# Performance work log

Hardware: AMD Instinct MI355X
Metric: run time of the kernel (lower is better)

The kernel has to match this reference:

```python
import jax, jax.numpy as jnp
import numpy as np

V_PER_MESH = 6596
HIDDEN = 128
# per-body-part clamp limits from the original module (parts 1..14)
LIMITS = jnp.array([0.04, 0.06, 0.04, 0.04, 0.02, 0.02, 0.04, 0.04,
                    0.03, 0.03, 0.02, 0.02, 0.01, 0.01], dtype=jnp.float32)


def setup_inputs() -> dict:
    key = jax.random.key(0)
    ks = jax.random.split(key, 16)
    B, V, H = 32, V_PER_MESH, HIDDEN
    N = B * V
    E = 3 * N
    inp = {}
    inp["verts"] = jax.random.normal(ks[0], (N, 3), jnp.float32)
    inp["normals"] = jax.random.normal(ks[1], (N, 3), jnp.float32)
    inp["anchor_v"] = jax.random.uniform(ks[2], (V, 3), jnp.float32)
    inp["edges"] = jax.random.randint(ks[3], (E, 2), 0, N)
    inp["part_id"] = jax.random.randint(ks[4], (V,), 0, 14)
    dims = [3, H + 3, H + 3]  # first gconv sees only vert normals (vert_feat_dim=0)
    i = 5
    for l, d in enumerate(dims):
        s = 1.0 / np.sqrt(d)
        inp[f"w0_{l}"] = jax.random.normal(ks[i], (d, H), jnp.float32) * s; i += 1
        inp[f"b0_{l}"] = jnp.zeros((H,), jnp.float32)
        inp[f"w1_{l}"] = jax.random.normal(ks[i], (d, H), jnp.float32) * s; i += 1
        inp[f"b1_{l}"] = jnp.zeros((H,), jnp.float32)
    inp["w_off"] = jax.random.normal(ks[i], (H + 3, 3), jnp.float32) * 0.01
    inp["b_off"] = jnp.zeros((3,), jnp.float32)
    return inp


def _forward(verts, normals, anchor_v, edges, part_id, layers, w_off, b_off):
    N = verts.shape[0]
    B = N // V_PER_MESH
    e0, e1 = edges[:, 0], edges[:, 1]
    feats = normals  # vert_pos_packed (verts_normals_packed), vert_feats=None
    for (w0, b0, w1, b1) in layers:
        x0 = feats @ w0 + b0            # [N,H] self transform
        x1 = feats @ w1 + b1            # [N,H] neighbor transform
        # undirected gather-scatter over mesh edges
        nbr = jnp.zeros_like(x0).at[e0].add(x1[e1]).at[e1].add(x1[e0])
        h = jax.nn.relu(x0 + nbr)       # vert_feats_nopos
        feats = jnp.concatenate([h, normals], axis=1)  # [N,H+3]
    deform = jnp.tanh(feats @ w_off + b_off)  # [N,3]
    # per-body-part clamp, vectorized: one limit per vertex, tiled over meshes
    lim = jnp.tile(LIMITS[part_id], B)[:, None]          # [N,1]
    clamped = jnp.clip(deform, -lim, lim)
    anchor = jnp.tile(anchor_v, (B, 1))                  # [N,3]
    new_verts = verts + clamped * anchor                 # offset_verts
    return new_verts, h


def reference(verts, normals, anchor_v, edges, part_id,
              w0_0, b0_0, w1_0, b1_0,
              w0_1, b0_1, w1_1, b1_1,
              w0_2, b0_2, w1_2, b1_2,
              w_off, b_off):
    layers = [(w0_0, b0_0, w1_0, b1_0),
              (w0_1, b0_1, w1_1, b1_1),
              (w0_2, b0_2, w1_2, b1_2)]
    return _forward(verts, normals, anchor_v, edges, part_id, layers, w_off, b_off)
```

## Files before the change

kernel.cpp:

```cpp
#include <hip/hip_runtime.h>

#define N_TOT 211072
#define V_MESH 6596
#define E_TOT 633216
#define CAP 32
#define KP 184
#define KSTEPS 5

typedef __attribute__((ext_vector_type(8))) short bf16x8;
typedef __attribute__((ext_vector_type(4))) float f32x4;

__constant__ float c_LIM[14] = {0.04f,0.06f,0.04f,0.04f,0.02f,0.02f,0.04f,0.04f,
                                0.03f,0.03f,0.02f,0.02f,0.01f,0.01f};

__device__ __forceinline__ unsigned f2bf(float f) {
    unsigned x = __float_as_uint(f);
    return (x + 0x7fffu + ((x >> 16) & 1u)) >> 16;
}
__device__ __forceinline__ float bflo(unsigned u) { return __uint_as_float(u << 16); }
__device__ __forceinline__ float bfhi(unsigned u) { return __uint_as_float(u & 0xffff0000u); }
__device__ __forceinline__ unsigned cvt_pk_bf16(float lo, float hi) {
    unsigned r;
    asm("v_cvt_pk_bf16_f32 %0, %1, %2" : "=v"(r) : "v"(lo), "v"(hi));
    return r;
}

__global__ __launch_bounds__(256) void fill_adj_kernel(const int* __restrict__ edges,
                                                       int* __restrict__ cnt,
                                                       int* __restrict__ adj) {
    int e = blockIdx.x * 256 + threadIdx.x;
    if (e >= E_TOT) return;
    int2 ed = ((const int2*)edges)[e];
    int p0 = atomicAdd(&cnt[ed.x], 1);
    if (p0 < CAP) adj[(size_t)ed.x * CAP + p0] = ed.y;
    int p1 = atomicAdd(&cnt[ed.y], 1);
    if (p1 < CAP) adj[(size_t)ed.y * CAP + p1] = ed.x;
}

__global__ __launch_bounds__(256) void pad_adj_kernel(const int* __restrict__ cnt,
                                                      int* __restrict__ adj) {
    int i = blockIdx.x * 256 + threadIdx.x;
    if (i >= N_TOT) return;
    int deg = cnt[i]; if (deg > CAP) deg = CAP;
    for (int k = deg; k < CAP; ++k) adj[(size_t)i * CAP + k] = N_TOT;
}

__global__ __launch_bounds__(256) void prep_nrm4_kernel(const float* __restrict__ normals,
                                                        float4* __restrict__ nrm4) {
    int i = blockIdx.x * 256 + threadIdx.x;
    if (i > N_TOT) return;
    float4 v = {0.f, 0.f, 0.f, 0.f};
    if (i < N_TOT) {
        v.x = normals[(size_t)i * 3 + 0];
        v.y = normals[(size_t)i * 3 + 1];
        v.z = normals[(size_t)i * 3 + 2];
    }
    nrm4[i] = v;
}

__global__ __launch_bounds__(256) void nsum_kernel(const float4* __restrict__ nrm4,
                                                   const int* __restrict__ cnt,
                                                   const int* __restrict__ adj,
                                                   float4* __restrict__ SS) {
    int i = blockIdx.x * 256 + threadIdx.x;
    if (i >= N_TOT) return;
    int deg = cnt[i]; if (deg > CAP) deg = CAP;
    const int4* a4 = (const int4*)(adj + (size_t)i * CAP);
    int4 A = a4[0], B = a4[1];
    float4 n0 = nrm4[A.x], n1 = nrm4[A.y], n2 = nrm4[A.z], n3 = nrm4[A.w];
    float4 m0 = nrm4[B.x], m1 = nrm4[B.y], m2 = nrm4[B.z], m3 = nrm4[B.w];
    float sx = ((n0.x + n1.x) + (n2.x + n3.x)) + ((m0.x + m1.x) + (m2.x + m3.x));
    float sy = ((n0.y + n1.y) + (n2.y + n3.y)) + ((m0.y + m1.y) + (m2.y + m3.y));
    float sz = ((n0.z + n1.z) + (n2.z + n3.z)) + ((m0.z + m1.z) + (m2.z + m3.z));
    for (int bq = 8; bq < deg; bq += 8) {
        int4 C = a4[bq / 4], D = a4[bq / 4 + 1];
        float4 p0 = nrm4[C.x], p1 = nrm4[C.y], p2 = nrm4[C.z], p3 = nrm4[C.w];
        float4 q0 = nrm4[D.x], q1 = nrm4[D.y], q2 = nrm4[D.z], q3 = nrm4[D.w];
        sx += ((p0.x + p1.x) + (p2.x + p3.x)) + ((q0.x + q1.x) + (q2.x + q3.x));
        sy += ((p0.y + p1.y) + (p2.y + p3.y)) + ((q0.y + q1.y) + (q2.y + q3.y));
        sz += ((p0.z + p1.z) + (p2.z + p3.z)) + ((q0.z + q1.z) + (q2.z + q3.z));
    }
    float4 out; out.x = sx; out.y = sy; out.z = sz; out.w = (float)deg;
    SS[i] = out;
}

__global__ __launch_bounds__(256) void conv_w_kernel(const float* __restrict__ w0,
                                                     const float* __restrict__ b0,
                                                     const float* __restrict__ w1,
                                                     const float* __restrict__ b1,
                                                     short* __restrict__ Wt,
                                                     float* __restrict__ bb) {
    int c = blockIdx.x;
    int k = threadIdx.x;
    const float* w = (c < 128) ? w0 : w1;
    int cc = c & 127;
    if (k < KP) {
        unsigned val = (k < 131) ? f2bf(w[(size_t)k * 128 + cc]) : 0u;
        Wt[(size_t)c * KP + k] = (short)val;
    }
    if (k == 0) bb[c] = (c < 128) ? b0[cc] : b1[cc];
}

__global__ __launch_bounds__(1024, 8) void fused1_kernel(const float4* __restrict__ nrm4,
                                                         const float4* __restrict__ SS,
                                                         const float* __restrict__ w0,
                                                         const float* __restrict__ b0,
                                                         const float* __restrict__ w1,
                                                         const float* __restrict__ b1,
                                                         const short* __restrict__ Wt,
                                                         const float* __restrict__ bb,
                                                         unsigned* __restrict__ xc_out) {
    __shared__ short tileA[16 * KP];
    __shared__ short tileC[16 * 256];
    __shared__ float wL[2][3][128];
    __shared__ float bL[2][128];

    int tid  = threadIdx.x;
    int w    = tid >> 6;
    int lane = tid & 63;
    int g    = lane >> 4;
    int ln   = lane & 15;
    int row0 = blockIdx.x * 16;
    int i    = row0 + w;

    if (tid < 768) {
        int mm = tid / 384, r = tid - mm * 384;
        (&wL[mm][0][0])[r] = (mm ? w1 : w0)[r];
    } else {
        int t2 = tid - 768;
        if (t2 < 256) bL[t2 >> 7][t2 & 127] = ((t2 >> 7) ? b1 : b0)[t2 & 127];
    }

    float4 self4 = nrm4[i];
    float4 S4 = SS[i];
    float degf = S4.w;
    __syncthreads();

    int c0 = 2 * lane, c1 = 2 * lane + 1;
    float h0 = bL[0][c0] + degf * bL[1][c0]
             + self4.x * wL[0][0][c0] + self4.y * wL[0][1][c0] + self4.z * wL[0][2][c0]
             + S4.x * wL[1][0][c0] + S4.y * wL[1][1][c0] + S4.z * wL[1][2][c0];
    float h1 = bL[0][c1] + degf * bL[1][c1]
             + self4.x * wL[0][0][c1] + self4.y * wL[0][1][c1] + self4.z * wL[0][2][c1]
             + S4.x * wL[1][0][c1] + S4.y * wL[1][1][c1] + S4.z * wL[1][2][c1];
    h0 = fmaxf(h0, 0.f);
    h1 = fmaxf(h1, 0.f);

    unsigned* tA32 = (unsigned*)tileA;
    tA32[w * (KP / 2) + lane] = cvt_pk_bf16(h0, h1);
    if (lane < 16) {
        unsigned v = (lane == 0) ? cvt_pk_bf16(self4.x, self4.y)
                   : (lane == 1) ? cvt_pk_bf16(self4.z, 0.f) : 0u;
        tA32[w * (KP / 2) + 64 + lane] = v;
    }
    __syncthreads();

    int cb = w * 16;
    float bv = bb[cb + ln];
    f32x4 acc = {bv, bv, bv, bv};
    #pragma unroll
    for (int kk = 0; kk < KSTEPS; ++kk) {
        bf16x8 bf = *(const bf16x8*)(Wt + (size_t)(cb + ln) * KP + kk * 32 + g * 8);
        bf16x8 af = *(const bf16x8*)(tileA + ln * KP + kk * 32 + g * 8);
        acc = __builtin_amdgcn_mfma_f32_16x16x32_bf16(af, bf, acc, 0, 0, 0);
    }
    #pragma unroll
    for (int j = 0; j < 4; ++j) {
        float po = __shfl_xor(acc[j], 1);
        if (!(ln & 1)) {
            unsigned pk = cvt_pk_bf16(acc[j], po);
            int dd = w * 8 + (ln >> 1);
            int row = g * 4 + j;
            ((unsigned*)tileC)[row * 128 + (dd ^ (g << 3))] = pk;
        }
    }
    __syncthreads();

    int key = (w >> 2) << 3;
    ushort4 v4 = *(const ushort4*)&((unsigned*)tileC)[w * 128 + ((2 * lane) ^ key)];
    ((ushort4*)(xc_out + (size_t)(row0 + w) * 128))[lane] = v4;
}

__global__ __launch_bounds__(1024, 8) void fused_kernel(const unsigned* __restrict__ xc_in,
                                                        const float4* __restrict__ nrm4,
                                                        const int* __restrict__ cnt,
                                                        const int* __restrict__ adj,
                                                        const short* __restrict__ Wt,
                                                        const float* __restrict__ bb,
                                                        unsigned* __restrict__ xc_out) {
    __shared__ short tileA[16 * KP];
    __shared__ short tileC[16 * 256];
    int tid  = threadIdx.x;
    int w    = tid >> 6;
    int lane = tid & 63;
    int g    = lane >> 4;
    int ln   = lane & 15;
    int row0 = blockIdx.x * 16;
    int i    = row0 + w;

    int deg0 = cnt[i];
    int jv = (lane < CAP) ? adj[(size_t)i * CAP + lane] : (int)N_TOT;

    const unsigned* x1b = xc_in + 64 + lane;
    unsigned u[8];
    #pragma unroll
    for (int q = 0; q < 8; ++q) {
        int j = __builtin_amdgcn_readlane(jv, q);
        u[q] = x1b[(size_t)j * 128];
    }
    unsigned selfu = xc_in[(size_t)i * 128 + lane];
    float4 self4 = nrm4[i];
    int cb = w * 16;
    float bv = bb[cb + ln];
    bf16x8 bfrag[KSTEPS];
    #pragma unroll
    for (int kk = 0; kk < KSTEPS; ++kk)
        bfrag[kk] = *(const bf16x8*)(Wt + (size_t)(cb + ln) * KP + kk * 32 + g * 8);

    float a0 = bflo(selfu), a1 = bfhi(selfu);
    float d0 = 0.f, d1 = 0.f;
    #pragma unroll
    for (int q = 0; q < 8; q += 2) {
        a0 += bflo(u[q]);     a1 += bfhi(u[q]);
        d0 += bflo(u[q + 1]); d1 += bfhi(u[q + 1]);
    }
    int deg = (deg0 > CAP) ? CAP : deg0;
    deg = __builtin_amdgcn_readfirstlane(deg);
    for (int bq = 8; bq < deg; bq += 8) {
        unsigned v[8];
        #pragma unroll
        for (int q = 0; q < 8; ++q) {
            int j = __builtin_amdgcn_readlane(jv, bq + q);
            v[q] = x1b[(size_t)j * 128];
        }
        #pragma unroll
        for (int q = 0; q < 8; q += 2) {
            a0 += bflo(v[q]);     a1 += bfhi(v[q]);
            d0 += bflo(v[q + 1]); d1 += bfhi(v[q + 1]);
        }
    }
    a0 = fmaxf(a0 + d0, 0.f);
    a1 = fmaxf(a1 + d1, 0.f);

    unsigned* tA32 = (unsigned*)tileA;
    tA32[w * (KP / 2) + lane] = cvt_pk_bf16(a0, a1);
    if (lane < 16) {
        unsigned v = (lane == 0) ? cvt_pk_bf16(self4.x, self4.y)
                   : (lane == 1) ? cvt_pk_bf16(self4.z, 0.f) : 0u;
        tA32[w * (KP / 2) + 64 + lane] = v;
    }
    __syncthreads();

    f32x4 acc = {bv, bv, bv, bv};
    #pragma unroll
    for (int kk = 0; kk < KSTEPS; ++kk) {
        bf16x8 af = *(const bf16x8*)(tileA + ln * KP + kk * 32 + g * 8);
        acc = __builtin_amdgcn_mfma_f32_16x16x32_bf16(af, bfrag[kk], acc, 0, 0, 0);
    }
    #pragma unroll
    for (int j = 0; j < 4; ++j) {
        float po = __shfl_xor(acc[j], 1);
        if (!(ln & 1)) {
            unsigned pk = cvt_pk_bf16(acc[j], po);
            int dd = w * 8 + (ln >> 1);
            int row = g * 4 + j;
            ((unsigned*)tileC)[row * 128 + (dd ^ (g << 3))] = pk;
        }
    }
    __syncthreads();

    int key = (w >> 2) << 3;
    ushort4 v4 = *(const ushort4*)&((unsigned*)tileC)[w * 128 + ((2 * lane) ^ key)];
    ((ushort4*)(xc_out + (size_t)(row0 + w) * 128))[lane] = v4;
}

__global__ __launch_bounds__(256) void final_fused_kernel(const unsigned* __restrict__ xc_in,
                                                          const int* __restrict__ cnt,
                                                          const int* __restrict__ adj,
                                                          const float* __restrict__ normals,
                                                          const float* __restrict__ verts,
                                                          const float* __restrict__ anchor_v,
                                                          const int* __restrict__ part_id,
                                                          const float* __restrict__ w_off,
                                                          const float* __restrict__ b_off,
                                                          float* __restrict__ hout,
                                                          float* __restrict__ out_verts) {
    __shared__ float wo[131 * 3];
    for (int t = threadIdx.x; t < 131 * 3; t += 256) wo[t] = w_off[t];
    __syncthreads();
    int tid  = threadIdx.x;
    int w    = tid >> 6;
    int lane = tid & 63;
    int i    = blockIdx.x * 4 + w;

    int deg0 = cnt[i];
    int jv = (lane < CAP) ? adj[(size_t)i * CAP + lane] : (int)N_TOT;
    unsigned selfu = xc_in[(size_t)i * 128 + lane];

    const unsigned* x1b = xc_in + 64 + lane;
    unsigned u[8];
    #pragma unroll
    for (int q = 0; q < 8; ++q) {
        int j = __builtin_amdgcn_readlane(jv, q);
        u[q] = x1b[(size_t)j * 128];
    }
    float a0 = bflo(selfu), a1 = bfhi(selfu);
    float d0 = 0.f, d1 = 0.f;
    #pragma unroll
    for (int q = 0; q < 8; q += 2) {
        a0 += bflo(u[q]);     a1 += bfhi(u[q]);
        d0 += bflo(u[q + 1]); d1 += bfhi(u[q + 1]);
    }
    int deg = (deg0 > CAP) ? CAP : deg0;
    deg = __builtin_amdgcn_readfirstlane(deg);
    for (int bq = 8; bq < deg; bq += 8) {
        unsigned v[8];
        #pragma unroll
        for (int q = 0; q < 8; ++q) {
            int j = __builtin_amdgcn_readlane(jv, bq + q);
            v[q] = x1b[(size_t)j * 128];
        }
        #pragma unroll
        for (int q = 0; q < 8; q += 2) {
            a0 += bflo(v[q]);     a1 += bfhi(v[q]);
            d0 += bflo(v[q + 1]); d1 += bfhi(v[q + 1]);
        }
    }
    a0 = fmaxf(a0 + d0, 0.f);
    a1 = fmaxf(a1 + d1, 0.f);

    float2 hv; hv.x = a0; hv.y = a1;
    ((float2*)(hout + (size_t)i * 128))[lane] = hv;

    int cA = 2 * lane, cB = 2 * lane + 1;
    float s0 = a0 * wo[cA * 3 + 0] + a1 * wo[cB * 3 + 0];
    float s1 = a0 * wo[cA * 3 + 1] + a1 * wo[cB * 3 + 1];
    float s2 = a0 * wo[cA * 3 + 2] + a1 * wo[cB * 3 + 2];
    #pragma unroll
    for (int dd = 32; dd; dd >>= 1) {
        s0 += __shfl_xor(s0, dd);
        s1 += __shfl_xor(s1, dd);
        s2 += __shfl_xor(s2, dd);
    }
    if (lane < 3) {
        int v = i % V_MESH;
        float n0 = normals[(size_t)i * 3 + 0];
        float n1 = normals[(size_t)i * 3 + 1];
        float n2 = normals[(size_t)i * 3 + 2];
        float s = (lane == 0) ? s0 : (lane == 1) ? s1 : s2;
        s += n0 * wo[128 * 3 + lane] + n1 * wo[129 * 3 + lane] + n2 * wo[130 * 3 + lane];
        s += b_off[lane];
        float dd2 = tanhf(s);
        float lim = c_LIM[part_id[v]];
        dd2 = fminf(fmaxf(dd2, -lim), lim);
        out_verts[(size_t)i * 3 + lane] =
            verts[(size_t)i * 3 + lane] + dd2 * anchor_v[(size_t)v * 3 + lane];
    }
}

extern "C" void kernel_launch(void* const* d_in, const int* in_sizes, int n_in,
                              void* d_out, int out_size, void* d_ws, size_t ws_size,
                              hipStream_t stream) {
    const float* verts    = (const float*)d_in[0];
    const float* normals  = (const float*)d_in[1];
    const float* anchor_v = (const float*)d_in[2];
    const int*   edges    = (const int*)d_in[3];
    const int*   part_id  = (const int*)d_in[4];
    const float* w0_0 = (const float*)d_in[5];
    const float* b0_0 = (const float*)d_in[6];
    const float* w1_0 = (const float*)d_in[7];
    const float* b1_0 = (const float*)d_in[8];
    const float* w0_1 = (const float*)d_in[9];
    const float* b0_1 = (const float*)d_in[10];
    const float* w1_1 = (const float*)d_in[11];
    const float* b1_1 = (const float*)d_in[12];
    const float* w0_2 = (const float*)d_in[13];
    const float* b0_2 = (const float*)d_in[14];
    const float* w1_2 = (const float*)d_in[15];
    const float* b1_2 = (const float*)d_in[16];
    const float* w_off = (const float*)d_in[17];
    const float* b_off = (const float*)d_in[18];

    float* out_verts = (float*)d_out;
    float* hout = (float*)d_out + (size_t)3 * N_TOT;

    unsigned* xcB = (unsigned*)d_out;

    char* p = (char*)d_ws;
    unsigned* xcA = (unsigned*)p;  p += (size_t)(N_TOT + 1) * 128 * 4;
    int*   cnt  = (int*)p;         p += (size_t)N_TOT * 4;
    int*   adj  = (int*)p;         p += (size_t)N_TOT * CAP * 4;
    short* Wt1  = (short*)p;       p += 256 * KP * 2;
    float* bb1  = (float*)p;       p += 256 * 4;
    short* Wt2  = (short*)p;       p += 256 * KP * 2;
    float* bb2  = (float*)p;       p += 256 * 4;
    float4* nrm4 = (float4*)p;     p += (size_t)(N_TOT + 1) * 16;
    float4* SS   = (float4*)p;     p += (size_t)N_TOT * 16;

    hipMemsetAsync(cnt, 0, (size_t)N_TOT * 4, stream);
    hipMemsetAsync(xcA + (size_t)N_TOT * 128, 0, 512, stream);
    hipMemsetAsync(xcB + (size_t)N_TOT * 128, 0, 512, stream);
    fill_adj_kernel<<<(E_TOT + 255) / 256, 256, 0, stream>>>(edges, cnt, adj);
    pad_adj_kernel<<<(N_TOT + 255) / 256, 256, 0, stream>>>(cnt, adj);
    prep_nrm4_kernel<<<(N_TOT + 256) / 256, 256, 0, stream>>>(normals, nrm4);
    conv_w_kernel<<<256, 256, 0, stream>>>(w0_1, b0_1, w1_1, b1_1, Wt1, bb1);
    conv_w_kernel<<<256, 256, 0, stream>>>(w0_2, b0_2, w1_2, b1_2, Wt2, bb2);
    nsum_kernel<<<(N_TOT + 255) / 256, 256, 0, stream>>>(nrm4, cnt, adj, SS);

    fused1_kernel<<<N_TOT / 16, 1024, 0, stream>>>(nrm4, SS, w0_0, b0_0, w1_0, b1_0,
                                                   Wt1, bb1, xcB);
    fused_kernel<<<N_TOT / 16, 1024, 0, stream>>>(xcB, nrm4, cnt, adj, Wt2, bb2, xcA);
    final_fused_kernel<<<N_TOT / 4, 256, 0, stream>>>(xcA, cnt, adj, normals, verts,
                                                      anchor_v, part_id, w_off, b_off,
                                                      hout, out_verts);
}
```

Measured before the change: 471.8 us.

## Aggregate-then-transform: store h instead of x0/x1, gather h before GEMM

Restructures each graph-conv layer to gather neighbor hidden features h (64 packed bf16 words per row) first and then run one GEMM over the concatenation of self and neighbor sums with K=256, instead of computing x0|x1 (128 words per row) and gathering x1. The normals part of the input is folded into per-column head terms: bias, degree times bias, normals and the neighbor-normal sums from SS. The final layer's GEMM is fused with the offset head, the tanh, the clamp and the vertex update. This halves the per-row bytes moved by the random neighbor gathers at the cost of a larger MFMA K dimension and an extra layer-wise GEMM in the last kernel.

```diff
diff --git a/kernel.cpp b/kernel.cpp
--- a/kernel.cpp
+++ b/kernel.cpp
@@ -4,8 +4,8 @@
 #define V_MESH 6596
 #define E_TOT 633216
 #define CAP 32
-#define KP 184
-#define KSTEPS 5
+#define KD 264
+#define KSTEPS 8
 
 typedef __attribute__((ext_vector_type(8))) short bf16x8;
 typedef __attribute__((ext_vector_type(4))) float f32x4;
@@ -84,53 +84,48 @@
     SS[i] = out;
 }
 
-__global__ __launch_bounds__(256) void conv_w_kernel(const float* __restrict__ w0,
-                                                     const float* __restrict__ b0,
-                                                     const float* __restrict__ w1,
-                                                     const float* __restrict__ b1,
-                                                     short* __restrict__ Wt,
-                                                     float* __restrict__ bb) {
+__global__ __launch_bounds__(256) void conv_w2_kernel(const float* __restrict__ w0,
+                                                      const float* __restrict__ b0,
+                                                      const float* __restrict__ w1,
+                                                      const float* __restrict__ b1,
+                                                      short* __restrict__ Wt,
+                                                      float4* __restrict__ hdA,
+                                                      float4* __restrict__ hdB) {
     int c = blockIdx.x;
-    int k = threadIdx.x;
-    const float* w = (c < 128) ? w0 : w1;
-    int cc = c & 127;
-    if (k < KP) {
-        unsigned val = (k < 131) ? f2bf(w[(size_t)k * 128 + cc]) : 0u;
-        Wt[(size_t)c * KP + k] = (short)val;
-    }
-    if (k == 0) bb[c] = (c < 128) ? b0[cc] : b1[cc];
-}
-
-__global__ __launch_bounds__(1024, 8) void fused1_kernel(const float4* __restrict__ nrm4,
-                                                         const float4* __restrict__ SS,
-                                                         const float* __restrict__ w0,
-                                                         const float* __restrict__ b0,
-                                                         const float* __restrict__ w1,
-                                                         const float* __restrict__ b1,
-                                                         const short* __restrict__ Wt,
-                                                         const float* __restrict__ bb,
-                                                         unsigned* __restrict__ xc_out) {
-    __shared__ short tileA[16 * KP];
-    __shared__ short tileC[16 * 256];
+    for (int k = threadIdx.x; k < KD; k += 256) {
+        unsigned val = 0u;
+        if (k < 128)      val = f2bf(w0[(size_t)k * 128 + c]);
+        else if (k < 256) val = f2bf(w1[(size_t)(k - 128) * 128 + c]);
+        Wt[(size_t)c * KD + k] = (short)val;
+    }
+    if (threadIdx.x == 0) {
+        hdA[c] = make_float4(b0[c], b1[c], w0[128 * 128 + c], w0[129 * 128 + c]);
+        hdB[c] = make_float4(w0[130 * 128 + c], w1[128 * 128 + c],
+                             w1[129 * 128 + c], w1[130 * 128 + c]);
+    }
+}
+
+__global__ __launch_bounds__(1024) void fused1_kernel(const float4* __restrict__ nrm4,
+                                                      const float4* __restrict__ SS,
+                                                      const float* __restrict__ w0,
+                                                      const float* __restrict__ b0,
+                                                      const float* __restrict__ w1,
+                                                      const float* __restrict__ b1,
+                                                      unsigned* __restrict__ hout) {
     __shared__ float wL[2][3][128];
     __shared__ float bL[2][128];
-
     int tid  = threadIdx.x;
     int w    = tid >> 6;
     int lane = tid & 63;
-    int g    = lane >> 4;
-    int ln   = lane & 15;
-    int row0 = blockIdx.x * 16;
-    int i    = row0 + w;
+    int i    = blockIdx.x * 16 + w;
 
     if (tid < 768) {
         int mm = tid / 384, r = tid - mm * 384;
         (&wL[mm][0][0])[r] = (mm ? w1 : w0)[r];
-    } else {
+    } else if (tid < 1024) {
         int t2 = tid - 768;
         if (t2 < 256) bL[t2 >> 7][t2 & 127] = ((t2 >> 7) ? b1 : b0)[t2 & 127];
     }
-
     float4 self4 = nrm4[i];
     float4 S4 = SS[i];
     float degf = S4.w;
@@ -143,218 +138,186 @@
     float h1 = bL[0][c1] + degf * bL[1][c1]
              + self4.x * wL[0][0][c1] + self4.y * wL[0][1][c1] + self4.z * wL[0][2][c1]
              + S4.x * wL[1][0][c1] + S4.y * wL[1][1][c1] + S4.z * wL[1][2][c1];
-    h0 = fmaxf(h0, 0.f);
-    h1 = fmaxf(h1, 0.f);
-
-    unsigned* tA32 = (unsigned*)tileA;
-    tA32[w * (KP / 2) + lane] = cvt_pk_bf16(h0, h1);
-    if (lane < 16) {
-        unsigned v = (lane == 0) ? cvt_pk_bf16(self4.x, self4.y)
-                   : (lane == 1) ? cvt_pk_bf16(self4.z, 0.f) : 0u;
-        tA32[w * (KP / 2) + 64 + lane] = v;
-    }
-    __syncthreads();
-
-    int cb = w * 16;
-    float bv = bb[cb + ln];
-    f32x4 acc = {bv, bv, bv, bv};
-    #pragma unroll
-    for (int kk = 0; kk < KSTEPS; ++kk) {
-        bf16x8 bf = *(const bf16x8*)(Wt + (size_t)(cb + ln) * KP + kk * 32 + g * 8);
-        bf16x8 af = *(const bf16x8*)(tileA + ln * KP + kk * 32 + g * 8);
-        acc = __builtin_amdgcn_mfma_f32_16x16x32_bf16(af, bf, acc, 0, 0, 0);
-    }
-    #pragma unroll
-    for (int j = 0; j < 4; ++j) {
-        float po = __shfl_xor(acc[j], 1);
-        if (!(ln & 1)) {
-            unsigned pk = cvt_pk_bf16(acc[j], po);
-            int dd = w * 8 + (ln >> 1);
-            int row = g * 4 + j;
-            ((unsigned*)tileC)[row * 128 + (dd ^ (g << 3))] = pk;
-        }
-    }
-    __syncthreads();
-
-    int key = (w >> 2) << 3;
-    ushort4 v4 = *(const ushort4*)&((unsigned*)tileC)[w * 128 + ((2 * lane) ^ key)];
-    ((ushort4*)(xc_out + (size_t)(row0 + w) * 128))[lane] = v4;
-}
-
-__global__ __launch_bounds__(1024, 8) void fused_kernel(const unsigned* __restrict__ xc_in,
+    hout[(size_t)i * 64 + lane] = cvt_pk_bf16(fmaxf(h0, 0.f), fmaxf(h1, 0.f));
+}
+
+template<int LAST>
+__global__ __launch_bounds__(512, 4) void fused2_kernel(const unsigned* __restrict__ hin,
                                                         const float4* __restrict__ nrm4,
+                                                        const float4* __restrict__ SS,
                                                         const int* __restrict__ cnt,
                                                         const int* __restrict__ adj,
                                                         const short* __restrict__ Wt,
-                                                        const float* __restrict__ bb,
-                                                        unsigned* __restrict__ xc_out) {
-    __shared__ short tileA[16 * KP];
-    __shared__ short tileC[16 * 256];
+                                                        const float4* __restrict__ hdA,
+                                                        const float4* __restrict__ hdB,
+                                                        unsigned* __restrict__ hnext,
+                                                        const float* __restrict__ verts,
+                                                        const float* __restrict__ anchor_v,
+                                                        const int* __restrict__ part_id,
+                                                        const float* __restrict__ w_off,
+                                                        const float* __restrict__ b_off,
+                                                        float* __restrict__ houtf,
+                                                        float* __restrict__ out_verts) {
+    __shared__ short tileA[16 * KD];
+    __shared__ unsigned tileC[16 * 64];
+    __shared__ float headL[16][8];
+    __shared__ float woL[131 * 3];
+    __shared__ float partL[8][16][3];
+
     int tid  = threadIdx.x;
     int w    = tid >> 6;
     int lane = tid & 63;
     int g    = lane >> 4;
     int ln   = lane & 15;
     int row0 = blockIdx.x * 16;
-    int i    = row0 + w;
-
-    int deg0 = cnt[i];
-    int jv = (lane < CAP) ? adj[(size_t)i * CAP + lane] : (int)N_TOT;
-
-    const unsigned* x1b = xc_in + 64 + lane;
-    unsigned u[8];
+    int rA   = 2 * w, rB = 2 * w + 1;
+    int iA   = row0 + rA, iB = row0 + rB;
+
+    if (LAST) {
+        for (int t = tid; t < 131 * 3; t += 512) woL[t] = w_off[t];
+    }
+
+    int node = (lane < 32) ? iA : iB;
+    int jv = adj[(size_t)node * CAP + (lane & 31)];
+    int degA = cnt[iA]; degA = (degA > CAP) ? CAP : degA;
+    int degB = cnt[iB]; degB = (degB > CAP) ? CAP : degB;
+    unsigned selfA = hin[(size_t)iA * 64 + lane];
+    unsigned selfB = hin[(size_t)iB * 64 + lane];
+    float4 nn = nrm4[node];
+    float4 sv = SS[node];
+    if ((lane & 31) == 0) {
+        int r = rA + (lane >> 5);
+        headL[r][0] = nn.x; headL[r][1] = nn.y; headL[r][2] = nn.z; headL[r][3] = sv.w;
+        headL[r][4] = sv.x; headL[r][5] = sv.y; headL[r][6] = sv.z; headL[r][7] = 0.f;
+    }
+
+    const unsigned* hb = hin + lane;
+    unsigned uA[8], uB[8];
     #pragma unroll
     for (int q = 0; q < 8; ++q) {
-        int j = __builtin_amdgcn_readlane(jv, q);
-        u[q] = x1b[(size_t)j * 128];
-    }
-    unsigned selfu = xc_in[(size_t)i * 128 + lane];
-    float4 self4 = nrm4[i];
-    int cb = w * 16;
-    float bv = bb[cb + ln];
-    bf16x8 bfrag[KSTEPS];
-    #pragma unroll
-    for (int kk = 0; kk < KSTEPS; ++kk)
-        bfrag[kk] = *(const bf16x8*)(Wt + (size_t)(cb + ln) * KP + kk * 32 + g * 8);
-
-    float a0 = bflo(selfu), a1 = bfhi(selfu);
-    float d0 = 0.f, d1 = 0.f;
-    #pragma unroll
-    for (int q = 0; q < 8; q += 2) {
-        a0 += bflo(u[q]);     a1 += bfhi(u[q]);
-        d0 += bflo(u[q + 1]); d1 += bfhi(u[q + 1]);
-    }
-    int deg = (deg0 > CAP) ? CAP : deg0;
-    deg = __builtin_amdgcn_readfirstlane(deg);
-    for (int bq = 8; bq < deg; bq += 8) {
+        int jA = __builtin_amdgcn_readlane(jv, q);
+        int jB = __builtin_amdgcn_readlane(jv, 32 + q);
+        uA[q] = hb[(size_t)jA * 64];
+        uB[q] = hb[(size_t)jB * 64];
+    }
+    float sA0 = 0.f, sA1 = 0.f, sB0 = 0.f, sB1 = 0.f;
+    #pragma unroll
+    for (int q = 0; q < 8; ++q) {
+        sA0 += bflo(uA[q]); sA1 += bfhi(uA[q]);
+        sB0 += bflo(uB[q]); sB1 += bfhi(uB[q]);
+    }
+    degA = __builtin_amdgcn_readfirstlane(degA);
+    degB = __builtin_amdgcn_readfirstlane(degB);
+    for (int bq = 8; bq < degA; bq += 8) {
         unsigned v[8];
         #pragma unroll
         for (int q = 0; q < 8; ++q) {
             int j = __builtin_amdgcn_readlane(jv, bq + q);
-            v[q] = x1b[(size_t)j * 128];
-        }
-        #pragma unroll
-        for (int q = 0; q < 8; q += 2) {
-            a0 += bflo(v[q]);     a1 += bfhi(v[q]);
-            d0 += bflo(v[q + 1]); d1 += bfhi(v[q + 1]);
-        }
-    }
-    a0 = fmaxf(a0 + d0, 0.f);
-    a1 = fmaxf(a1 + d1, 0.f);
-
-    unsigned* tA32 = (unsigned*)tileA;
-    tA32[w * (KP / 2) + lane] = cvt_pk_bf16(a0, a1);
-    if (lane < 16) {
-        unsigned v = (lane == 0) ? cvt_pk_bf16(self4.x, self4.y)
-                   : (lane == 1) ? cvt_pk_bf16(self4.z, 0.f) : 0u;
-        tA32[w * (KP / 2) + 64 + lane] = v;
+            v[q] = hb[(size_t)j * 64];
+        }
+        #pragma unroll
+        for (int q = 0; q < 8; ++q) { sA0 += bflo(v[q]); sA1 += bfhi(v[q]); }
+    }
+    for (int bq = 8; bq < degB; bq += 8) {
+        unsigned v[8];
+        #pragma unroll
+        for (int q = 0; q < 8; ++q) {
+            int j = __builtin_amdgcn_readlane(jv, 32 + bq + q);
+            v[q] = hb[(size_t)j * 64];
+        }
+        #pragma unroll
+        for (int q = 0; q < 8; ++q) { sB0 += bflo(v[q]); sB1 += bfhi(v[q]); }
+    }
+
+    unsigned* tA = (unsigned*)tileA;
+    tA[rA * 132 + lane]      = selfA;
+    tA[rB * 132 + lane]      = selfB;
+    tA[rA * 132 + 64 + lane] = cvt_pk_bf16(sA0, sA1);
+    tA[rB * 132 + 64 + lane] = cvt_pk_bf16(sB0, sB1);
+    if (lane < 4) {
+        tA[rA * 132 + 128 + lane] = 0u;
+        tA[rB * 132 + 128 + lane] = 0u;
     }
     __syncthreads();
 
-    f32x4 acc = {bv, bv, bv, bv};
+    int cb = w * 16, c = cb + ln;
+    float4 hA = hdA[c], hB = hdB[c];
+    bf16x8 bfrag[KSTEPS];
+    #pragma unroll
+    for (int kk = 0; kk < KSTEPS; ++kk)
+        bfrag[kk] = *(const bf16x8*)(Wt + (size_t)c * KD + kk * 32 + g * 8);
+
+    f32x4 acc;
+    #pragma unroll
+    for (int j = 0; j < 4; ++j) {
+        int r = g * 4 + j;
+        acc[j] = hA.x + headL[r][3] * hA.y
+               + headL[r][0] * hA.z + headL[r][1] * hA.w + headL[r][2] * hB.x
+               + headL[r][4] * hB.y + headL[r][5] * hB.z + headL[r][6] * hB.w;
+    }
     #pragma unroll
     for (int kk = 0; kk < KSTEPS; ++kk) {
-        bf16x8 af = *(const bf16x8*)(tileA + ln * KP + kk * 32 + g * 8);
+        bf16x8 af = *(const bf16x8*)(tileA + ln * KD + kk * 32 + g * 8);
         acc = __builtin_amdgcn_mfma_f32_16x16x32_bf16(af, bfrag[kk], acc, 0, 0, 0);
     }
     #pragma unroll
-    for (int j = 0; j < 4; ++j) {
-        float po = __shfl_xor(acc[j], 1);
-        if (!(ln & 1)) {
-            unsigned pk = cvt_pk_bf16(acc[j], po);
-            int dd = w * 8 + (ln >> 1);
-            int row = g * 4 + j;
-            ((unsigned*)tileC)[row * 128 + (dd ^ (g << 3))] = pk;
-        }
-    }
-    __syncthreads();
-
-    int key = (w >> 2) << 3;
-    ushort4 v4 = *(const ushort4*)&((unsigned*)tileC)[w * 128 + ((2 * lane) ^ key)];
-    ((ushort4*)(xc_out + (size_t)(row0 + w) * 128))[lane] = v4;
-}
-
-__global__ __launch_bounds__(256) void final_fused_kernel(const unsigned* __restrict__ xc_in,
-                                                          const int* __restrict__ cnt,
-                                                          const int* __restrict__ adj,
-                                                          const float* __restrict__ normals,
-                                                          const float* __restrict__ verts,
-                                                          const float* __restrict__ anchor_v,
-                                                          const int* __restrict__ part_id,
-                                                          const float* __restrict__ w_off,
-                                                          const float* __restrict__ b_off,
-                                                          float* __restrict__ hout,
-                                                          float* __restrict__ out_verts) {
-    __shared__ float wo[131 * 3];
-    for (int t = threadIdx.x; t < 131 * 3; t += 256) wo[t] = w_off[t];
-    __syncthreads();
-    int tid  = threadIdx.x;
-    int w    = tid >> 6;
-    int lane = tid & 63;
-    int i    = blockIdx.x * 4 + w;
-
-    int deg0 = cnt[i];
-    int jv = (lane < CAP) ? adj[(size_t)i * CAP + lane] : (int)N_TOT;
-    unsigned selfu = xc_in[(size_t)i * 128 + lane];
-
-    const unsigned* x1b = xc_in + 64 + lane;
-    unsigned u[8];
-    #pragma unroll
-    for (int q = 0; q < 8; ++q) {
-        int j = __builtin_amdgcn_readlane(jv, q);
-        u[q] = x1b[(size_t)j * 128];
-    }
-    float a0 = bflo(selfu), a1 = bfhi(selfu);
-    float d0 = 0.f, d1 = 0.f;
-    #pragma unroll
-    for (int q = 0; q < 8; q += 2) {
-        a0 += bflo(u[q]);     a1 += bfhi(u[q]);
-        d0 += bflo(u[q + 1]); d1 += bfhi(u[q + 1]);
-    }
-    int deg = (deg0 > CAP) ? CAP : deg0;
-    deg = __builtin_amdgcn_readfirstlane(deg);
-    for (int bq = 8; bq < deg; bq += 8) {
-        unsigned v[8];
-        #pragma unroll
-        for (int q = 0; q < 8; ++q) {
-            int j = __builtin_amdgcn_readlane(jv, bq + q);
-            v[q] = x1b[(size_t)j * 128];
-        }
-        #pragma unroll
-        for (int q = 0; q < 8; q += 2) {
-            a0 += bflo(v[q]);     a1 += bfhi(v[q]);
-            d0 += bflo(v[q + 1]); d1 += bfhi(v[q + 1]);
-        }
-    }
-    a0 = fmaxf(a0 + d0, 0.f);
-    a1 = fmaxf(a1 + d1, 0.f);
-
-    float2 hv; hv.x = a0; hv.y = a1;
-    ((float2*)(hout + (size_t)i * 128))[lane] = hv;
-
-    int cA = 2 * lane, cB = 2 * lane + 1;
-    float s0 = a0 * wo[cA * 3 + 0] + a1 * wo[cB * 3 + 0];
-    float s1 = a0 * wo[cA * 3 + 1] + a1 * wo[cB * 3 + 1];
-    float s2 = a0 * wo[cA * 3 + 2] + a1 * wo[cB * 3 + 2];
-    #pragma unroll
-    for (int dd = 32; dd; dd >>= 1) {
-        s0 += __shfl_xor(s0, dd);
-        s1 += __shfl_xor(s1, dd);
-        s2 += __shfl_xor(s2, dd);
-    }
-    if (lane < 3) {
-        int v = i % V_MESH;
-        float n0 = normals[(size_t)i * 3 + 0];
-        float n1 = normals[(size_t)i * 3 + 1];
-        float n2 = normals[(size_t)i * 3 + 2];
-        float s = (lane == 0) ? s0 : (lane == 1) ? s1 : s2;
-        s += n0 * wo[128 * 3 + lane] + n1 * wo[129 * 3 + lane] + n2 * wo[130 * 3 + lane];
-        s += b_off[lane];
-        float dd2 = tanhf(s);
-        float lim = c_LIM[part_id[v]];
-        dd2 = fminf(fmaxf(dd2, -lim), lim);
-        out_verts[(size_t)i * 3 + lane] =
-            verts[(size_t)i * 3 + lane] + dd2 * anchor_v[(size_t)v * 3 + lane];
+    for (int j = 0; j < 4; ++j) acc[j] = fmaxf(acc[j], 0.f);
+
+    if (!LAST) {
+        #pragma unroll
+        for (int j = 0; j < 4; ++j) {
+            float po = __shfl_xor(acc[j], 1);
+            if (!(ln & 1)) {
+                unsigned pk = cvt_pk_bf16(acc[j], po);
+                int r = g * 4 + j;
+                int d = (cb + ln) >> 1;
+                tileC[r * 64 + (d ^ ((r & 3) << 3))] = pk;
+            }
+        }
+        __syncthreads();
+        int r2 = 2 * w + (lane >> 5);
+        int d2 = (lane & 31) * 2;
+        int key = (r2 & 3) << 3;
+        uint2 v2 = *(const uint2*)&tileC[r2 * 64 + (d2 ^ key)];
+        *(uint2*)(hnext + (size_t)(row0 + r2) * 64 + d2) = v2;
+    } else {
+        #pragma unroll
+        for (int j = 0; j < 4; ++j) {
+            int r = g * 4 + j;
+            houtf[(size_t)(row0 + r) * 128 + c] = acc[j];
+        }
+        #pragma unroll
+        for (int j = 0; j < 4; ++j) {
+            int r = g * 4 + j;
+            float p0 = acc[j] * woL[c * 3 + 0];
+            float p1 = acc[j] * woL[c * 3 + 1];
+            float p2 = acc[j] * woL[c * 3 + 2];
+            #pragma unroll
+            for (int d = 1; d < 16; d <<= 1) {
+                p0 += __shfl_xor(p0, d);
+                p1 += __shfl_xor(p1, d);
+                p2 += __shfl_xor(p2, d);
+            }
+            if (ln == 0) {
+                partL[w][r][0] = p0; partL[w][r][1] = p1; partL[w][r][2] = p2;
+            }
+        }
+        __syncthreads();
+        if (tid < 48) {
+            int r = tid / 3, t = tid - r * 3;
+            int i = row0 + r;
+            float s = 0.f;
+            #pragma unroll
+            for (int ww = 0; ww < 8; ++ww) s += partL[ww][r][t];
+            s += headL[r][0] * woL[128 * 3 + t] + headL[r][1] * woL[129 * 3 + t]
+               + headL[r][2] * woL[130 * 3 + t] + b_off[t];
+            float dd = tanhf(s);
+            int v = i % V_MESH;
+            float lim = c_LIM[part_id[v]];
+            dd = fminf(fmaxf(dd, -lim), lim);
+            out_verts[(size_t)i * 3 + t] =
+                verts[(size_t)i * 3 + t] + dd * anchor_v[(size_t)v * 3 + t];
+        }
     }
 }
 
@@ -382,35 +345,37 @@
     const float* b_off = (const float*)d_in[18];
 
     float* out_verts = (float*)d_out;
-    float* hout = (float*)d_out + (size_t)3 * N_TOT;
-
-    unsigned* xcB = (unsigned*)d_out;
+    float* houtf = (float*)d_out + (size_t)3 * N_TOT;
 
     char* p = (char*)d_ws;
-    unsigned* xcA = (unsigned*)p;  p += (size_t)(N_TOT + 1) * 128 * 4;
-    int*   cnt  = (int*)p;         p += (size_t)N_TOT * 4;
-    int*   adj  = (int*)p;         p += (size_t)N_TOT * CAP * 4;
-    short* Wt1  = (short*)p;       p += 256 * KP * 2;
-    float* bb1  = (float*)p;       p += 256 * 4;
-    short* Wt2  = (short*)p;       p += 256 * KP * 2;
-    float* bb2  = (float*)p;       p += 256 * 4;
+    unsigned* h1 = (unsigned*)p;   p += (size_t)(N_TOT + 1) * 64 * 4;
+    unsigned* h2 = (unsigned*)p;   p += (size_t)(N_TOT + 1) * 64 * 4;
+    int*    cnt  = (int*)p;        p += (size_t)N_TOT * 4;
+    int*    adj  = (int*)p;        p += (size_t)N_TOT * CAP * 4;
+    short*  Wt1  = (short*)p;      p += 128 * KD * 2;
+    short*  Wt2  = (short*)p;      p += 128 * KD * 2;
+    float4* hdA1 = (float4*)p;     p += 128 * 16;
+    float4* hdB1 = (float4*)p;     p += 128 * 16;
+    float4* hdA2 = (float4*)p;     p += 128 * 16;
+    float4* hdB2 = (float4*)p;     p += 128 * 16;
     float4* nrm4 = (float4*)p;     p += (size_t)(N_TOT + 1) * 16;
     float4* SS   = (float4*)p;     p += (size_t)N_TOT * 16;
 
     hipMemsetAsync(cnt, 0, (size_t)N_TOT * 4, stream);
-    hipMemsetAsync(xcA + (size_t)N_TOT * 128, 0, 512, stream);
-    hipMemsetAsync(xcB + (size_t)N_TOT * 128, 0, 512, stream);
+    hipMemsetAsync(h1 + (size_t)N_TOT * 64, 0, 256, stream);
+    hipMemsetAsync(h2 + (size_t)N_TOT * 64, 0, 256, stream);
     fill_adj_kernel<<<(E_TOT + 255) / 256, 256, 0, stream>>>(edges, cnt, adj);
     pad_adj_kernel<<<(N_TOT + 255) / 256, 256, 0, stream>>>(cnt, adj);
     prep_nrm4_kernel<<<(N_TOT + 256) / 256, 256, 0, stream>>>(normals, nrm4);
-    conv_w_kernel<<<256, 256, 0, stream>>>(w0_1, b0_1, w1_1, b1_1, Wt1, bb1);
-    conv_w_kernel<<<256, 256, 0, stream>>>(w0_2, b0_2, w1_2, b1_2, Wt2, bb2);
+    conv_w2_kernel<<<128, 256, 0, stream>>>(w0_1, b0_1, w1_1, b1_1, Wt1, hdA1, hdB1);
+    conv_w2_kernel<<<128, 256, 0, stream>>>(w0_2, b0_2, w1_2, b1_2, Wt2, hdA2, hdB2);
     nsum_kernel<<<(N_TOT + 255) / 256, 256, 0, stream>>>(nrm4, cnt, adj, SS);
 
-    fused1_kernel<<<N_TOT / 16, 1024, 0, stream>>>(nrm4, SS, w0_0, b0_0, w1_0, b1_0,
-                                                   Wt1, bb1, xcB);
-    fused_kernel<<<N_TOT / 16, 1024, 0, stream>>>(xcB, nrm4, cnt, adj, Wt2, bb2, xcA);
-    final_fused_kernel<<<N_TOT / 4, 256, 0, stream>>>(xcA, cnt, adj, normals, verts,
-                                                      anchor_v, part_id, w_off, b_off,
-                                                      hout, out_verts);
-}
+    fused1_kernel<<<N_TOT / 16, 1024, 0, stream>>>(nrm4, SS, w0_0, b0_0, w1_0, b1_0, h1);
+    fused2_kernel<0><<<N_TOT / 16, 512, 0, stream>>>(h1, nrm4, SS, cnt, adj, Wt1, hdA1, hdB1,
+                                                     h2, nullptr, nullptr, nullptr, nullptr,
+                                                     nullptr, nullptr, nullptr);
+    fused2_kernel<1><<<N_TOT / 16, 512, 0, stream>>>(h2, nrm4, SS, cnt, adj, Wt2, hdA2, hdB2,
+                                                     nullptr, verts, anchor_v, part_id,
+                                                     w_off, b_off, houtf, out_verts);
+}
```

Result: faster. 409.4 us (-13.2%).
